# Kernel tuning notes

Hardware: AMD Instinct MI355X
Metric: run time of the kernel (lower is better)

Reference implementation:

```python
import jax, jax.numpy as jnp
import numpy as np

B, S, D, H, DFF, NL, VOCAB, SRC = 16, 128, 768, 12, 3072, 6, 32000, 256


def _pe_table():
    pos = np.arange(S)[:, None].astype(np.float32)
    div = np.exp(np.arange(0, D, 2).astype(np.float32) * (-np.log(10000.0) / D))
    pe = np.zeros((S, D), np.float32)
    pe[:, 0::2] = np.sin(pos * div)
    pe[:, 1::2] = np.cos(pos * div)
    return jnp.asarray(pe)


def _ln(x, a, b, eps=1e-6):
    m = jnp.mean(x, axis=-1, keepdims=True)
    v = jnp.mean((x - m) ** 2, axis=-1, keepdims=True)
    return a * (x - m) / jnp.sqrt(v + eps) + b


def _mha(q_in, k_in, v_in, mask, Wq, bq, Wk, bk, Wv, bv, Wo, bo):
    Bq, Sq, Dm = q_in.shape
    Sk = k_in.shape[1]
    dk = Dm // H
    q = (q_in @ Wq + bq).reshape(Bq, Sq, H, dk).transpose(0, 2, 1, 3)
    k = (k_in @ Wk + bk).reshape(Bq, Sk, H, dk).transpose(0, 2, 1, 3)
    v = (v_in @ Wv + bv).reshape(Bq, Sk, H, dk).transpose(0, 2, 1, 3)
    s = jnp.einsum('bhqd,bhkd->bhqk', q, k) / jnp.sqrt(jnp.float32(dk))
    if mask is not None:
        s = jnp.where(mask == 0, jnp.float32(-1e9), s)
    a = jax.nn.softmax(s, axis=-1)
    o = jnp.einsum('bhqk,bhkd->bhqd', a, v).transpose(0, 2, 1, 3).reshape(Bq, Sq, Dm)
    return o @ Wo + bo


def _combined_mask(trg):
    # Vectorized, faithful replica of create_combined_mask (incl. its cumulative
    # cross-batch zeroing: for j in 0..B-2, if padding_start[j]!=0 zero rows
    # >= padding_start[j] of ALL batches b >= j).
    b, s = trg.shape
    is_pad = (trg == 0)
    haspad = jnp.any(is_pad, axis=1)
    start = jnp.where(haspad, jnp.argmax(is_pad, axis=1), 0)  # first pad idx, 0 if none
    c = jnp.where(start == 0, s + 1, start)                   # sentinel = never cut
    cmin = jax.lax.cummin(c)
    r = cmin[jnp.minimum(jnp.arange(b), b - 2)]               # effective cutoff per batch
    look = jnp.tril(jnp.ones((s, s), jnp.float32))
    keep = (jnp.arange(s)[None, :] < r[:, None]).astype(jnp.float32)  # (B,S) rows kept
    return (look[None] * keep[:, :, None])[:, None]           # (B,1,S,S)


def setup_inputs():
    key = jax.random.key(0)
    ks = jax.random.split(key, 16)
    tok = jax.random.randint(ks[0], (B, S), 1, VOCAB)
    lens = jax.random.randint(ks[1], (B,), S // 2, S + 1)
    trg = jnp.where(jnp.arange(S)[None, :] < lens[:, None], tok, 0).astype(jnp.int32)
    e_outputs = jax.random.normal(ks[2], (B, SRC, D), dtype=jnp.float32)
    src_mask = jax.random.randint(ks[3], (B, 1, 1, SRC), 0, 2).at[..., 0].set(1).astype(jnp.int32)
    w = lambda k, shape: (jax.random.normal(k, shape) * 0.02).astype(jnp.float32)
    emb = (jax.random.normal(ks[4], (VOCAB, D)) * 0.1).astype(jnp.float32).at[0].set(0.0)
    return {
        'trg': trg, 'e_outputs': e_outputs, 'src_mask': src_mask,
        'emb': emb,
        'y_param': jax.random.normal(ks[5], (S, D), dtype=jnp.float32),
        'pe_alpha': jnp.float32(1.0),
        'Wq': w(ks[6], (NL, 3, D, D)), 'Wk': w(ks[7], (NL, 3, D, D)),
        'Wv': w(ks[8], (NL, 3, D, D)), 'Wo': w(ks[9], (NL, 3, D, D)),
        'bq': jnp.zeros((NL, 3, D)), 'bk': jnp.zeros((NL, 3, D)),
        'bv': jnp.zeros((NL, 3, D)), 'bo': jnp.zeros((NL, 3, D)),
        'W1': w(ks[10], (NL, D, DFF)), 'b1': jnp.zeros((NL, DFF)),
        'W2': w(ks[11], (NL, DFF, D)), 'b2': jnp.zeros((NL, D)),
        'ln_a': jnp.ones((NL, 5, D)), 'ln_b': jnp.zeros((NL, 5, D)),
        'final_a': jnp.ones((D,)), 'final_b': jnp.zeros((D,)),
    }


def reference(trg, e_outputs, src_mask, emb, y_param, pe_alpha, Wq, Wk, Wv, Wo,
              bq, bk, bv, bo, W1, b1, W2, b2, ln_a, ln_b, final_a, final_b):
    x = emb[trg] + pe_alpha * _pe_table()            # embedding + scaled PE
    y = jnp.broadcast_to(y_param, (trg.shape[0],) + y_param.shape)
    trg_mask = _combined_mask(trg)
    for i in range(Wq.shape[0]):
        x2 = _ln(x, ln_a[i, 0], ln_b[i, 0])
        x = x + _mha(x2, x2, x2, trg_mask, Wq[i, 0], bq[i, 0], Wk[i, 0], bk[i, 0], Wv[i, 0], bv[i, 0], Wo[i, 0], bo[i, 0])
        y2 = _ln(y, ln_a[i, 1], ln_b[i, 1])
        y = y + _mha(y2, e_outputs, e_outputs, src_mask, Wq[i, 1], bq[i, 1], Wk[i, 1], bk[i, 1], Wv[i, 1], bv[i, 1], Wo[i, 1], bo[i, 1])
        x2 = _ln(x, ln_a[i, 2], ln_b[i, 2])
        y3 = _ln(y, ln_a[i, 3], ln_b[i, 3])
        x = x + _mha(x2, y3, y3, None, Wq[i, 2], bq[i, 2], Wk[i, 2], bk[i, 2], Wv[i, 2], bv[i, 2], Wo[i, 2], bo[i, 2])
        x2 = _ln(x, ln_a[i, 4], ln_b[i, 4])
        x = x + jnp.maximum(x2 @ W1[i] + b1[i], 0.0) @ W2[i] + b2[i]
    return _ln(x, final_a, final_b)
```

## Files before the change

### kernel.cpp

```cpp
#include <hip/hip_runtime.h>
#include <math.h>

#define BB 16
#define SS 128
#define DD 768
#define HH 12
#define DKK 64
#define DFFF 3072
#define NLL 6
#define SRCC 256

typedef short bf16x8 __attribute__((ext_vector_type(8)));
typedef float f32x4 __attribute__((ext_vector_type(4)));
typedef unsigned short us8 __attribute__((ext_vector_type(8)));
typedef unsigned short us4 __attribute__((ext_vector_type(4)));

__device__ __forceinline__ unsigned short f2bf(float f) {
  unsigned int u = __builtin_bit_cast(unsigned int, f);
  u = (u + 0x7fff + ((u >> 16) & 1)) >> 16;
  return (unsigned short)u;
}

#define GLOADLDS16(gp, lp)                                              \
  __builtin_amdgcn_global_load_lds(                                     \
      (const __attribute__((address_space(1))) void*)(gp),              \
      (__attribute__((address_space(3))) void*)(lp), 16, 0, 0)

__global__ void embjoint_k(const int* __restrict__ trg, const float* __restrict__ emb,
                           const float* __restrict__ alpha,
                           const float* __restrict__ yp,
                           float* __restrict__ x, float* __restrict__ y) {
  int idx = blockIdx.x * blockDim.x + threadIdx.x;
  int c = idx % (DD / 4);
  int r = idx / (DD / 4);
  if (r >= BB * SS) return;
  int s = r % SS;
  if (blockIdx.y == 0) {
    float al = alpha[0];
    float4 e = *(const float4*)(emb + (size_t)trg[r] * DD + c * 4);
    float coef = -logf(10000.0f) / (float)DD;
    float div0 = expf((float)(4 * c) * coef);
    float div1 = expf((float)(4 * c + 2) * coef);
    float s0, c0, s1, c1;
    sincosf((float)s * div0, &s0, &c0);
    sincosf((float)s * div1, &s1, &c1);
    float4 o;
    o.x = e.x + al * s0; o.y = e.y + al * c0;
    o.z = e.z + al * s1; o.w = e.w + al * c1;
    *(float4*)(x + (size_t)r * DD + c * 4) = o;
  } else {
    *(float4*)(y + (size_t)r * DD + c * 4) = *(const float4*)(yp + (size_t)s * DD + c * 4);
  }
}

__global__ void mb_k(const int* __restrict__ trg, int* __restrict__ rbuf,
                     const float* __restrict__ bq, const float* __restrict__ bk,
                     const float* __restrict__ bv, float* __restrict__ bqkv1,
                     float* __restrict__ bkv2, float* __restrict__ bqkv3) {
  int t = threadIdx.x;
  if (blockIdx.x == 0) {
    __shared__ int first[BB];
    if (t < BB) first[t] = 0x7fffffff;
    __syncthreads();
    int b = t >> 4, p0 = (t & 15) * 8;
    int loc = 0x7fffffff;
#pragma unroll
    for (int i = 0; i < 8; i++) {
      if (trg[b * SS + p0 + i] == 0) { loc = p0 + i; break; }
    }
    atomicMin(&first[b], loc);
    __syncthreads();
    if (t == 0) {
      int cmin = 0x7fffffff;
      int cm[BB];
      for (int bb = 0; bb < BB; bb++) {
        int start = (first[bb] == 0x7fffffff) ? 0 : first[bb];
        int c = (start == 0) ? (SS + 1) : start;
        cmin = min(cmin, c);
        cm[bb] = cmin;
      }
      for (int bb = 0; bb < BB; bb++) rbuf[bb] = cm[min(bb, BB - 2)];
    }
    return;
  }
  int i = (blockIdx.x - 1) * 256 + t;
  if (i >= NLL * 6144) return;
  int l = i / 6144, j = i - l * 6144;
  if (j < 2304) {
    int s = j / 768, c = j - s * 768;
    const float* src = (s == 0) ? bq : (s == 1 ? bk : bv);
    bqkv1[l * 2304 + j] = src[(l * 3 + 0) * 768 + c];
  } else if (j < 3840) {
    int jj = j - 2304;
    int s = jj / 768, c = jj - s * 768;
    bkv2[l * 1536 + jj] = ((s == 0) ? bk : bv)[(l * 3 + 1) * 768 + c];
  } else {
    int jj = j - 3840;
    int s = jj / 768, c = jj - s * 768;
    const float* src = (s == 0) ? bq : (s == 1 ? bk : bv);
    bqkv3[l * 2304 + jj] = src[(l * 3 + 2) * 768 + c];
  }
}

__global__ __launch_bounds__(256) void ln_k(const float* __restrict__ x,
                                            const float* __restrict__ ga,
                                            const float* __restrict__ gb,
                                            float* __restrict__ out) {
  __shared__ float sm[8];
  int row = blockIdx.x;
  int t = threadIdx.x;
  const float* xr = x + (size_t)row * DD;
  float v0 = xr[t], v1 = xr[t + 256], v2 = xr[t + 512];
  float s = v0 + v1 + v2;
#pragma unroll
  for (int o = 32; o > 0; o >>= 1) s += __shfl_down(s, o);
  if ((t & 63) == 0) sm[t >> 6] = s;
  __syncthreads();
  float mean = (sm[0] + sm[1] + sm[2] + sm[3]) * (1.0f / (float)DD);
  float d0 = v0 - mean, d1 = v1 - mean, d2 = v2 - mean;
  float q = d0 * d0 + d1 * d1 + d2 * d2;
#pragma unroll
  for (int o = 32; o > 0; o >>= 1) q += __shfl_down(q, o);
  if ((t & 63) == 0) sm[4 + (t >> 6)] = q;
  __syncthreads();
  float var = (sm[4] + sm[5] + sm[6] + sm[7]) * (1.0f / (float)DD);
  float inv = 1.0f / sqrtf(var + 1e-6f);
  float* orow = out + (size_t)row * DD;
  orow[t]       = ga[t] * d0 * inv + gb[t];
  orow[t + 256] = ga[t + 256] * d1 * inv + gb[t + 256];
  orow[t + 512] = ga[t + 512] * d2 * inv + gb[t + 512];
}

__device__ __forceinline__ void lnb_body(const float* __restrict__ xr,
                                         const float* __restrict__ ga,
                                         const float* __restrict__ gb,
                                         unsigned short* __restrict__ orow,
                                         float* sm, int t) {
  float v0 = xr[t], v1 = xr[t + 256], v2 = xr[t + 512];
  float s = v0 + v1 + v2;
#pragma unroll
  for (int o = 32; o > 0; o >>= 1) s += __shfl_down(s, o);
  if ((t & 63) == 0) sm[t >> 6] = s;
  __syncthreads();
  float mean = (sm[0] + sm[1] + sm[2] + sm[3]) * (1.0f / (float)DD);
  float d0 = v0 - mean, d1 = v1 - mean, d2 = v2 - mean;
  float q = d0 * d0 + d1 * d1 + d2 * d2;
#pragma unroll
  for (int o = 32; o > 0; o >>= 1) q += __shfl_down(q, o);
  if ((t & 63) == 0) sm[4 + (t >> 6)] = q;
  __syncthreads();
  float var = (sm[4] + sm[5] + sm[6] + sm[7]) * (1.0f / (float)DD);
  float inv = 1.0f / sqrtf(var + 1e-6f);
  orow[t]       = f2bf(ga[t] * d0 * inv + gb[t]);
  orow[t + 256] = f2bf(ga[t + 256] * d1 * inv + gb[t + 256]);
  orow[t + 512] = f2bf(ga[t + 512] * d2 * inv + gb[t + 512]);
}

__global__ __launch_bounds__(256) void lnb_k(const float* __restrict__ x,
                                             const float* __restrict__ ga,
                                             const float* __restrict__ gb,
                                             unsigned short* __restrict__ out) {
  __shared__ float sm[8];
  int row = blockIdx.x;
  lnb_body(x + (size_t)row * DD, ga, gb, out + (size_t)row * DD, sm, threadIdx.x);
}

__global__ __launch_bounds__(256) void lnb2_k(const float* __restrict__ x,
                                              const float* __restrict__ y,
                                              const float* __restrict__ gax,
                                              const float* __restrict__ gbx,
                                              const float* __restrict__ gay,
                                              const float* __restrict__ gby,
                                              unsigned short* __restrict__ ox,
                                              unsigned short* __restrict__ oy) {
  __shared__ float sm[8];
  int row = blockIdx.x;
  if (row < BB * SS)
    lnb_body(x + (size_t)row * DD, gax, gbx, ox + (size_t)row * DD, sm, threadIdx.x);
  else {
    row -= BB * SS;
    lnb_body(y + (size_t)row * DD, gay, gby, oy + (size_t)row * DD, sm, threadIdx.x);
  }
}

__device__ __forceinline__ void tr_tile64(const float* __restrict__ s,
                                          unsigned short* __restrict__ d,
                                          int K, int N, int k0, int n0,
                                          float (*tl)[69], int t) {
#pragma unroll
  for (int i = 0; i < 4; i++) {
    int c = t + i * 256;
    int row = c >> 4, c4 = (c & 15) * 4;
    float4 v = *(const float4*)(s + (size_t)(k0 + row) * N + n0 + c4);
    tl[row][c4 + 0] = v.x; tl[row][c4 + 1] = v.y;
    tl[row][c4 + 2] = v.z; tl[row][c4 + 3] = v.w;
  }
  __syncthreads();
#pragma unroll
  for (int i = 0; i < 2; i++) {
    int c = t + i * 256;
    int n = c >> 3, kc = c & 7;
    us8 o;
#pragma unroll
    for (int j = 0; j < 8; j++) o[j] = f2bf(tl[kc * 8 + j][n]);
    *(us8*)(d + (size_t)(n0 + n) * K + k0 + kc * 8) = o;
  }
}

__global__ __launch_bounds__(256) void wtx_k(
    const float* __restrict__ Wq, const float* __restrict__ Wk,
    const float* __restrict__ Wv, const float* __restrict__ Wo,
    const float* __restrict__ W1, const float* __restrict__ W2,
    const float* __restrict__ e_out,
    unsigned short* __restrict__ wqkv1A, unsigned short* __restrict__ wq2A,
    unsigned short* __restrict__ wkv2A, unsigned short* __restrict__ wqkv3A,
    unsigned short* __restrict__ wotA,
    unsigned short* __restrict__ w1tA, unsigned short* __restrict__ w2tA,
    unsigned short* __restrict__ eob) {
  __shared__ float tl[64][69];
  const size_t M1 = (size_t)DD * DD;
  int bid = blockIdx.x;
  int t = threadIdx.x;
  if (bid < 10368) {
    int mat = bid / 144, rem = bid % 144;
    int kt = rem / 12, nt = rem % 12;
    int l = mat / 12, m = mat % 12;
    size_t s3 = (size_t)l * 3 * M1;
    const float* s;
    unsigned short* d;
    switch (m) {
      case 0:  s = Wq + s3;          d = wqkv1A + l * 3 * M1;          break;
      case 1:  s = Wk + s3;          d = wqkv1A + l * 3 * M1 + M1;     break;
      case 2:  s = Wv + s3;          d = wqkv1A + l * 3 * M1 + 2 * M1; break;
      case 3:  s = Wq + s3 + M1;     d = wq2A + l * M1;                break;
      case 4:  s = Wk + s3 + M1;     d = wkv2A + l * 2 * M1;           break;
      case 5:  s = Wv + s3 + M1;     d = wkv2A + l * 2 * M1 + M1;      break;
      case 6:  s = Wq + s3 + 2 * M1; d = wqkv3A + l * 3 * M1;          break;
      case 7:  s = Wk + s3 + 2 * M1; d = wqkv3A + l * 3 * M1 + M1;     break;
      case 8:  s = Wv + s3 + 2 * M1; d = wqkv3A + l * 3 * M1 + 2 * M1; break;
      case 9:  s = Wo + s3;          d = wotA + l * 3 * M1;            break;
      case 10: s = Wo + s3 + M1;     d = wotA + l * 3 * M1 + M1;       break;
      default: s = Wo + s3 + 2 * M1; d = wotA + l * 3 * M1 + 2 * M1;   break;
    }
    tr_tile64(s, d, DD, DD, kt * 64, nt * 64, tl, t);
  } else if (bid < 13824) {
    int idx = bid - 10368;
    int l = idx / 576, rem = idx % 576;
    int kt = rem / 48, nt = rem % 48;
    tr_tile64(W1 + (size_t)l * DD * DFFF, w1tA + (size_t)l * DD * DFFF,
              DD, DFFF, kt * 64, nt * 64, tl, t);
  } else if (bid < 17280) {
    int idx = bid - 13824;
    int l = idx / 576, rem = idx % 576;
    int kt = rem / 12, nt = rem % 12;
    tr_tile64(W2 + (size_t)l * DFFF * DD, w2tA + (size_t)l * DFFF * DD,
              DFFF, DD, kt * 64, nt * 64, tl, t);
  } else {
    size_t base = (size_t)(bid - 17280) * 2048 + (size_t)t * 8;
    float4 a = *(const float4*)(e_out + base);
    float4 b = *(const float4*)(e_out + base + 4);
    us8 o;
    o[0] = f2bf(a.x); o[1] = f2bf(a.y); o[2] = f2bf(a.z); o[3] = f2bf(a.w);
    o[4] = f2bf(b.x); o[5] = f2bf(b.y); o[6] = f2bf(b.z); o[7] = f2bf(b.w);
    *(us8*)(eob + base) = o;
  }
}

#define GEMM_BODY64(BM, A, Bt, m0, n0, KK)                                    \
  constexpr int FM = (BM) / 32;                                               \
  constexpr int HB = (BM) / 2;                                                \
  int wave = t >> 6, lane = t & 63;                                           \
  int wm = wave >> 1, wn = wave & 1;                                          \
  int l15 = lane & 15, lhi = lane >> 4;                                       \
  f32x4 acc[FM][2] = {};                                                      \
  int aRow = t >> 2, aC8 = (t & 3) * 8;                                       \
  const unsigned short* Ab = (A) + (size_t)(m0) * (KK) + aC8;                 \
  const unsigned short* Bb = (Bt) + (size_t)(n0) * (KK) + aC8;                \
  int aOff0 = (wm * HB + l15) * 32 + lhi * 8;                                 \
  int bOff0 = (wn * 32 + l15) * 32 + lhi * 8;                                 \
  for (int k0 = 0; k0 < (KK); k0 += 64) {                                     \
    _Pragma("unroll")                                                         \
    for (int p = 0; p < 2; p++) {                                             \
      _Pragma("unroll")                                                       \
      for (int h = 0; h < (BM) / 64; h++)                                     \
        GLOADLDS16(Ab + (size_t)(h * 64 + aRow) * (KK) + k0 + p * 32,         \
                   As + p * ((BM) * 32) + h * 2048 + wave * 512);             \
      GLOADLDS16(Bb + (size_t)aRow * (KK) + k0 + p * 32,                      \
                 Bs + p * 2048 + wave * 512);                                 \
    }                                                                         \
    __syncthreads();                                                          \
    _Pragma("unroll")                                                         \
    for (int p = 0; p < 2; p++) {                                             \
      bf16x8 aF[FM], bF[2];                                                   \
      _Pragma("unroll")                                                       \
      for (int fm = 0; fm < FM; fm++)                                         \
        aF[fm] = *(const bf16x8*)(As + p * ((BM) * 32) + aOff0 + fm * 16 * 32);\
      _Pragma("unroll")                                                       \
      for (int fn = 0; fn < 2; fn++)                                          \
        bF[fn] = *(const bf16x8*)(Bs + p * 2048 + bOff0 + fn * 16 * 32);      \
      _Pragma("unroll")                                                       \
      for (int fm = 0; fm < FM; fm++)                                         \
        _Pragma("unroll")                                                     \
        for (int fn = 0; fn < 2; fn++)                                        \
          acc[fm][fn] = __builtin_amdgcn_mfma_f32_16x16x32_bf16(              \
              aF[fm], bF[fn], acc[fm][fn], 0, 0, 0);                          \
    }                                                                         \
    __syncthreads();                                                          \
  }                                                                           \
  int lcol = l15, lrow4 = lhi * 4;

__device__ __forceinline__ void hm_store(unsigned short* hd, int sh, int vt,
                                         int rowb, int colr, const f32x4& a,
                                         float bv) {
  int hh = colr >> 6, dd = colr & 63;
  int bb = rowb >> sh, ssb = rowb & ((1 << sh) - 1);
  if (vt) {
    size_t idx = (((size_t)bb * HH + hh) * 64 + dd) * (size_t)(1 << sh) + ssb;
    us4 pk;
#pragma unroll
    for (int r = 0; r < 4; r++) pk[r] = f2bf(a[r] + bv);
    *(us4*)(hd + idx) = pk;
  } else {
    size_t base = ((((size_t)bb * HH + hh) << sh) + ssb) * 64 + dd;
#pragma unroll
    for (int r = 0; r < 4; r++) hd[base + (size_t)r * 64] = f2bf(a[r] + bv);
  }
}

template <int BM>
__global__ __launch_bounds__(256) void mgemm_k(
    const unsigned short* __restrict__ A0, const unsigned short* __restrict__ A1,
    const unsigned short* __restrict__ Bt, const float* __restrict__ bias,
    const float* __restrict__ res, void* __restrict__ C,
    unsigned short* __restrict__ hd0, unsigned short* __restrict__ hd1,
    unsigned short* __restrict__ hd2,
    int sh0, int sh1, int sh2, int M, int N, int K, int flags, int vtbits) {
  __shared__ unsigned short As[2 * BM * 32];
  __shared__ unsigned short Bs[2 * 64 * 32];
  int t = threadIdx.x;
  int m0 = blockIdx.y * BM, n0 = blockIdx.x * 64;
  int seg = n0 / 768;
  const unsigned short* A = (seg == 0) ? A0 : A1;
  GEMM_BODY64(BM, A, Bt, m0, n0, K)
  bool hm = (flags & 4) != 0;
  unsigned short* hd = nullptr;
  int sh = 0, segBase = seg * 768, vtseg = 0;
  if (hm) {
    hd = (seg == 0) ? hd0 : (seg == 1 ? hd1 : hd2);
    sh = (seg == 0) ? sh0 : (seg == 1 ? sh1 : sh2);
    vtseg = (vtbits >> seg) & 1;
  }
#pragma unroll
  for (int fm = 0; fm < FM; fm++) {
#pragma unroll
    for (int fn = 0; fn < 2; fn++) {
      int col = n0 + wn * 32 + fn * 16 + lcol;
      float bv = bias[col];
      int rowb = m0 + wm * HB + fm * 16 + lrow4;
      if (hm) {
        hm_store(hd, sh, vtseg, rowb, col - segBase, acc[fm][fn], bv);
      } else {
#pragma unroll
        for (int r = 0; r < 4; r++) {
          int row = rowb + r;
          float v = acc[fm][fn][r] + bv;
          size_t idx = (size_t)row * N + col;
          if (res) v += res[idx];
          if (flags & 1) v = fmaxf(v, 0.f);
          if (flags & 2) ((unsigned short*)C)[idx] = f2bf(v);
          else ((float*)C)[idx] = v;
        }
      }
    }
  }
}

__global__ __launch_bounds__(256) void kv2all_k(
    const unsigned short* __restrict__ eob, const unsigned short* __restrict__ wkv2A,
    const float* __restrict__ bkv2,
    unsigned short* __restrict__ khb2A, unsigned short* __restrict__ vthb2A) {
  __shared__ unsigned short As[2 * 128 * 32];
  __shared__ unsigned short Bs[2 * 64 * 32];
  const size_t M1 = (size_t)DD * DD;
  const size_t KVS = (size_t)BB * HH * SRCC * DKK;
  int t = threadIdx.x;
  int flat = blockIdx.x;
  int nf = (flat & 7) * 576 + (flat >> 3);
  int bx = nf % 24;
  int rem = nf / 24;
  int by = rem & 31;
  int l = rem >> 5;
  int m0 = by * 128, n0 = bx * 64;
  const unsigned short* Bt = wkv2A + (size_t)l * 2 * M1;
  const float* bias = bkv2 + l * 1536;
  GEMM_BODY64(128, eob, Bt, m0, n0, 768)
  int seg = n0 / 768;
  unsigned short* hd = (seg == 0) ? khb2A + (size_t)l * KVS : vthb2A + (size_t)l * KVS;
  int segBase = seg * 768;
#pragma unroll
  for (int fm = 0; fm < FM; fm++) {
#pragma unroll
    for (int fn = 0; fn < 2; fn++) {
      int col = n0 + wn * 32 + fn * 16 + lcol;
      int rowb = m0 + wm * HB + fm * 16 + lrow4;
      hm_store(hd, 8, seg, rowb, col - segBase, acc[fm][fn], bias[col]);
    }
  }
}

__global__ __launch_bounds__(256) void qkvq_k(
    const unsigned short* __restrict__ x2b, const unsigned short* __restrict__ y1b,
    const unsigned short* __restrict__ Bqkv, const unsigned short* __restrict__ Bq2,
    const float* __restrict__ bias1, const float* __restrict__ bias2,
    unsigned short* __restrict__ qhb, unsigned short* __restrict__ khb,
    unsigned short* __restrict__ vthb, unsigned short* __restrict__ qhb2) {
  __shared__ unsigned short As[2 * 128 * 32];
  __shared__ unsigned short Bs[2 * 64 * 32];
  int t = threadIdx.x;
  int bid = blockIdx.x;
  bool j1 = bid >= 576;
  int bx, by;
  const unsigned short *A, *Bt;
  const float* bias;
  if (!j1) { bx = bid % 36; by = bid / 36; A = x2b; Bt = Bqkv; bias = bias1; }
  else { int b2 = bid - 576; bx = b2 % 12; by = b2 / 12; A = y1b; Bt = Bq2; bias = bias2; }
  int m0 = by * 128, n0 = bx * 64;
  GEMM_BODY64(128, A, Bt, m0, n0, 768)
  int seg = j1 ? 0 : (n0 / 768);
  unsigned short* hd = j1 ? qhb2 : (seg == 0 ? qhb : (seg == 1 ? khb : vthb));
  int vt = (!j1 && seg == 2) ? 1 : 0;
  int segBase = seg * 768;
#pragma unroll
  for (int fm = 0; fm < FM; fm++) {
#pragma unroll
    for (int fn = 0; fn < 2; fn++) {
      int col = n0 + wn * 32 + fn * 16 + lcol;
      int rowb = m0 + wm * HB + fm * 16 + lrow4;
      hm_store(hd, 7, vt, rowb, col - segBase, acc[fm][fn], bias[col]);
    }
  }
}

__global__ __launch_bounds__(256) void wob_k(
    const unsigned short* __restrict__ ctx1b, const unsigned short* __restrict__ ctx2b,
    const unsigned short* __restrict__ Bt0, const unsigned short* __restrict__ Bt1,
    const float* __restrict__ bo0, const float* __restrict__ bo1,
    float* __restrict__ x, float* __restrict__ y) {
  __shared__ unsigned short As[2 * 64 * 32];
  __shared__ unsigned short Bs[2 * 64 * 32];
  int t = threadIdx.x;
  int bid = blockIdx.x;
  bool j1 = bid >= 384;
  int b2 = j1 ? bid - 384 : bid;
  int bx = b2 % 12, by = b2 / 12;
  const unsigned short* A = j1 ? ctx2b : ctx1b;
  const unsigned short* Bt = j1 ? Bt1 : Bt0;
  const float* bias = j1 ? bo1 : bo0;
  float* C = j1 ? y : x;
  int m0 = by * 64, n0 = bx * 64;
  GEMM_BODY64(64, A, Bt, m0, n0, 768)
#pragma unroll
  for (int fm = 0; fm < FM; fm++) {
#pragma unroll
    for (int fn = 0; fn < 2; fn++) {
      int col = n0 + wn * 32 + fn * 16 + lcol;
      float bv = bias[col];
      int rowb = m0 + wm * HB + fm * 16 + lrow4;
#pragma unroll
      for (int r = 0; r < 4; r++) {
        size_t idx = (size_t)(rowb + r) * DD + col;
        C[idx] += acc[fm][fn][r] + bv;
      }
    }
  }
}

template <int SK>
__device__ __forceinline__ void attn_body(
    const unsigned short* __restrict__ qh, const unsigned short* __restrict__ kh,
    const unsigned short* __restrict__ vth, unsigned short* __restrict__ ctxb,
    int mode, const int* __restrict__ rbuf, const int* __restrict__ smask,
    unsigned short* __restrict__ kvb, unsigned short* __restrict__ pbuf,
    int qhalf, int h, int b) {
  constexpr int NPH = SK / 128;
  constexpr int NF = SK / 16;
  int t = threadIdx.x;
  int wave = t >> 6, lane = t & 63;
  int l15 = lane & 15, lhi = lane >> 4;
  int qrow0 = qhalf * 64 + wave * 16;
  size_t bh = (size_t)b * HH + h;
  bf16x8 aQ[2];
#pragma unroll
  for (int ks = 0; ks < 2; ks++)
    aQ[ks] = *(const bf16x8*)(qh + (bh * SS + qrow0 + l15) * 64 + ks * 32 + lhi * 8);
  f32x4 accS[NF] = {};
  const unsigned short* kbase = kh + bh * SK * 64;
  for (int ph = 0; ph < NPH; ph++) {
    if (ph) __syncthreads();
    {
      int c0 = t * 4;
#pragma unroll
      for (int i = 0; i < 4; i++) {
        int c = c0 + i, row = c >> 3, co = (c & 7) * 8;
        *(us8*)&kvb[row * 72 + co] = *(const us8*)(kbase + (size_t)(ph * 128 + row) * 64 + co);
      }
    }
    __syncthreads();
#pragma unroll
    for (int kf = 0; kf < 8; kf++) {
      int gf = ph * 8 + kf;
#pragma unroll
      for (int ks = 0; ks < 2; ks++) {
        bf16x8 bK = *(const bf16x8*)(&kvb[(kf * 16 + l15) * 72 + ks * 32 + lhi * 8]);
        accS[gf] = __builtin_amdgcn_mfma_f32_16x16x32_bf16(aQ[ks], bK, accS[gf], 0, 0, 0);
      }
    }
  }
  int rcut = (mode == 0) ? rbuf[b] : 0;
#pragma unroll
  for (int r = 0; r < 4; r++) {
    int qg = qrow0 + lhi * 4 + r;
    float mx = -3.4e38f;
#pragma unroll
    for (int gf = 0; gf < NF; gf++) {
      int k = gf * 16 + l15;
      float s = accS[gf][r] * 0.125f;
      bool keep = true;
      if (mode == 0) keep = (k <= qg) && (qg < rcut);
      else if (mode == 1) keep = (smask[b * SRCC + k] != 0);
      s = keep ? s : -1e9f;
      accS[gf][r] = s;
      mx = fmaxf(mx, s);
    }
#pragma unroll
    for (int o = 1; o < 16; o <<= 1) mx = fmaxf(mx, __shfl_xor(mx, o));
    float sum = 0.f;
#pragma unroll
    for (int gf = 0; gf < NF; gf++) {
      float e = expf(accS[gf][r] - mx);
      accS[gf][r] = e;
      sum += e;
    }
#pragma unroll
    for (int o = 1; o < 16; o <<= 1) sum += __shfl_xor(sum, o);
    float rinv = 1.0f / sum;
#pragma unroll
    for (int gf = 0; gf < NF; gf++) accS[gf][r] *= rinv;
  }
#pragma unroll
  for (int gf = 0; gf < NF; gf++) {
#pragma unroll
    for (int r = 0; r < 4; r++) {
      int ql = wave * 16 + lhi * 4 + r;
      pbuf[ql * (SK + 8) + gf * 16 + l15] = f2bf(accS[gf][r]);
    }
  }
  __syncthreads();
  f32x4 accO[4] = {};
  const unsigned short* vbase = vth + bh * 64 * SK;
  for (int ph = 0; ph < NPH; ph++) {
    if (ph) __syncthreads();
    {
      int c0 = t * 4;
#pragma unroll
      for (int i = 0; i < 4; i++) {
        int c = c0 + i, row = c >> 4, co = (c & 15) * 8;
        *(us8*)&kvb[row * 136 + co] = *(const us8*)(vbase + (size_t)row * SK + ph * 128 + co);
      }
    }
    __syncthreads();
#pragma unroll
    for (int ks = 0; ks < 4; ks++) {
      bf16x8 aP = *(const bf16x8*)(&pbuf[(wave * 16 + l15) * (SK + 8) + ph * 128 + ks * 32 + lhi * 8]);
#pragma unroll
      for (int nf = 0; nf < 4; nf++) {
        bf16x8 bV = *(const bf16x8*)(&kvb[(nf * 16 + l15) * 136 + ks * 32 + lhi * 8]);
        accO[nf] = __builtin_amdgcn_mfma_f32_16x16x32_bf16(aP, bV, accO[nf], 0, 0, 0);
      }
    }
  }
#pragma unroll
  for (int nf = 0; nf < 4; nf++) {
#pragma unroll
    for (int r = 0; r < 4; r++) {
      int qg = qrow0 + lhi * 4 + r;
      ctxb[((size_t)b * SS + qg) * DD + h * 64 + nf * 16 + l15] = f2bf(accO[nf][r]);
    }
  }
}

template <int SK>
__global__ __launch_bounds__(256) void attn3_k(const unsigned short* __restrict__ qh,
                                               const unsigned short* __restrict__ kh,
                                               const unsigned short* __restrict__ vth,
                                               unsigned short* __restrict__ ctxb, int mode,
                                               const int* __restrict__ rbuf,
                                               const int* __restrict__ smask) {
  __shared__ unsigned short kvb[128 * 72];
  __shared__ unsigned short pbuf[64 * (SK + 8)];
  attn_body<SK>(qh, kh, vth, ctxb, mode, rbuf, smask, kvb, pbuf,
                blockIdx.x, blockIdx.y, blockIdx.z);
}

__global__ __launch_bounds__(256) void attnboth_k(
    const unsigned short* __restrict__ qh1, const unsigned short* __restrict__ kh1,
    const unsigned short* __restrict__ vth1,
    const unsigned short* __restrict__ qh2, const unsigned short* __restrict__ kh2,
    const unsigned short* __restrict__ vth2,
    unsigned short* __restrict__ ctx1b, unsigned short* __restrict__ ctx2b,
    const int* __restrict__ rbuf, const int* __restrict__ smask) {
  __shared__ unsigned short kvb[128 * 72];
  __shared__ unsigned short pbuf[64 * (SRCC + 8)];
  int bid = blockIdx.x;
  if (bid < 384) {
    int qhalf = bid & 1, rest = bid >> 1;
    int h = rest % HH, b = rest / HH;
    attn_body<SRCC>(qh2, kh2, vth2, ctx2b, 1, nullptr, smask, kvb, pbuf, qhalf, h, b);
  } else {
    int b2 = bid - 384;
    int qhalf = b2 & 1, rest = b2 >> 1;
    int h = rest % HH, b = rest / HH;
    attn_body<SS>(qh1, kh1, vth1, ctx1b, 0, rbuf, nullptr, kvb, pbuf, qhalf, h, b);
  }
}

extern "C" void kernel_launch(void* const* d_in, const int* in_sizes, int n_in,
                              void* d_out, int out_size, void* d_ws, size_t ws_size,
                              hipStream_t stream) {
  const int*   trg   = (const int*)d_in[0];
  const float* e_out = (const float*)d_in[1];
  const int*   smask = (const int*)d_in[2];
  const float* emb   = (const float*)d_in[3];
  const float* ypar  = (const float*)d_in[4];
  const float* alpha = (const float*)d_in[5];
  const float* Wq = (const float*)d_in[6];
  const float* Wk = (const float*)d_in[7];
  const float* Wv = (const float*)d_in[8];
  const float* Wo = (const float*)d_in[9];
  const float* bq = (const float*)d_in[10];
  const float* bk = (const float*)d_in[11];
  const float* bv = (const float*)d_in[12];
  const float* bo = (const float*)d_in[13];
  const float* W1 = (const float*)d_in[14];
  const float* b1 = (const float*)d_in[15];
  const float* W2 = (const float*)d_in[16];
  const float* b2 = (const float*)d_in[17];
  const float* lna = (const float*)d_in[18];
  const float* lnbp = (const float*)d_in[19];
  const float* fa = (const float*)d_in[20];
  const float* fb = (const float*)d_in[21];
  float* out = (float*)d_out;

  float* ws = (float*)d_ws;
  size_t off = 0;
  auto alloc = [&](size_t n) { float* p = ws + off; off += n; return p; };
  const size_t M1 = (size_t)DD * DD;
  const size_t KVS = (size_t)BB * HH * SRCC * DKK;
  int* rbuf  = (int*)alloc(64);
  float* x   = alloc((size_t)BB * SS * DD);
  float* y   = alloc((size_t)BB * SS * DD);
  float* bqkv1 = alloc((size_t)NLL * 2304);
  float* bkv2  = alloc((size_t)NLL * 1536);
  float* bqkv3 = alloc((size_t)NLL * 2304);
  unsigned short* qhb   = (unsigned short*)alloc((size_t)BB * HH * SS * DKK / 2);
  unsigned short* qhb2  = (unsigned short*)alloc((size_t)BB * HH * SS * DKK / 2);
  unsigned short* khb   = (unsigned short*)alloc((size_t)BB * HH * SS * DKK / 2);
  unsigned short* vthb  = (unsigned short*)alloc((size_t)BB * HH * SS * DKK / 2);
  unsigned short* khb2A  = (unsigned short*)alloc((size_t)NLL * KVS / 2);
  unsigned short* vthb2A = (unsigned short*)alloc((size_t)NLL * KVS / 2);
  unsigned short* x2b   = (unsigned short*)alloc((size_t)BB * SS * DD / 2);
  unsigned short* y3b   = (unsigned short*)alloc((size_t)BB * SS * DD / 2);
  unsigned short* ctx1b = (unsigned short*)alloc((size_t)BB * SS * DD / 2);
  unsigned short* ctx2b = (unsigned short*)alloc((size_t)BB * SS * DD / 2);
  unsigned short* midb  = (unsigned short*)alloc((size_t)BB * SS * DFFF / 2);
  unsigned short* eob   = (unsigned short*)alloc((size_t)BB * SRCC * DD / 2);
  unsigned short* wqkv1A = (unsigned short*)alloc((size_t)NLL * 3 * M1 / 2);
  unsigned short* wq2A   = (unsigned short*)alloc((size_t)NLL * M1 / 2);
  unsigned short* wkv2A  = (unsigned short*)alloc((size_t)NLL * 2 * M1 / 2);
  unsigned short* wqkv3A = (unsigned short*)alloc((size_t)NLL * 3 * M1 / 2);
  unsigned short* wotA   = (unsigned short*)alloc((size_t)NLL * 3 * M1 / 2);
  unsigned short* w1tA   = (unsigned short*)alloc((size_t)NLL * DD * DFFF / 2);
  unsigned short* w2tA   = (unsigned short*)alloc((size_t)NLL * DFFF * DD / 2);
  if (ws_size < off * sizeof(float)) return;

  embjoint_k<<<dim3((BB * SS * (DD / 4) + 255) / 256, 2), 256, 0, stream>>>(
      trg, emb, alpha, ypar, x, y);
  mb_k<<<1 + (NLL * 6144 + 255) / 256, 256, 0, stream>>>(trg, rbuf, bq, bk, bv,
                                                         bqkv1, bkv2, bqkv3);
  wtx_k<<<18816, 256, 0, stream>>>(Wq, Wk, Wv, Wo, W1, W2, e_out,
                                   wqkv1A, wq2A, wkv2A, wqkv3A, wotA, w1tA, w2tA, eob);
  kv2all_k<<<4608, 256, 0, stream>>>(eob, wkv2A, bkv2, khb2A, vthb2A);

  auto MG128 = [&](const unsigned short* A0, const unsigned short* A1, int M, int K,
                   const unsigned short* Bt, int N, const float* bias, const float* res,
                   void* C, unsigned short* h0, unsigned short* h1, unsigned short* h2,
                   int s0, int s1, int s2, int flags, int vtb) {
    mgemm_k<128><<<dim3(N / 64, M / 128), 256, 0, stream>>>(A0, A1, Bt, bias, res, C,
                                                            h0, h1, h2, s0, s1, s2, M, N, K, flags, vtb);
  };
  auto MG64 = [&](const unsigned short* A0, int M, int K,
                  const unsigned short* Bt, int N, const float* bias, const float* res,
                  void* C, unsigned short* h0, int s0, int flags, int vtb) {
    mgemm_k<64><<<dim3(N / 64, M / 64), 256, 0, stream>>>(A0, A0, Bt, bias, res, C,
                                                          h0, nullptr, nullptr, s0, 0, 0, M, N, K, flags, vtb);
  };
  const dim3 agrid(SS / 64, HH, BB);

  for (int l = 0; l < NLL; l++) {
    const float* lA = lna + (size_t)l * 5 * DD;
    const float* lB = lnbp + (size_t)l * 5 * DD;
    lnb2_k<<<2 * BB * SS, 256, 0, stream>>>(x, y, lA, lB, lA + DD, lB + DD, x2b, y3b);
    qkvq_k<<<768, 256, 0, stream>>>(x2b, y3b, wqkv1A + l * 3 * M1, wq2A + l * M1,
                                    bqkv1 + l * 2304, bq + ((size_t)l * 3 + 1) * DD,
                                    qhb, khb, vthb, qhb2);
    attnboth_k<<<768, 256, 0, stream>>>(qhb, khb, vthb,
                                        qhb2, khb2A + l * KVS, vthb2A + l * KVS,
                                        ctx1b, ctx2b, rbuf, smask);
    wob_k<<<768, 256, 0, stream>>>(ctx1b, ctx2b, wotA + l * 3 * M1, wotA + l * 3 * M1 + M1,
                                   bo + (size_t)l * 3 * DD, bo + ((size_t)l * 3 + 1) * DD, x, y);
    lnb2_k<<<2 * BB * SS, 256, 0, stream>>>(x, y, lA + 2 * DD, lB + 2 * DD,
                                            lA + 3 * DD, lB + 3 * DD, x2b, y3b);
    MG128(x2b, y3b, BB * SS, DD, wqkv3A + l * 3 * M1, 2304, bqkv3 + l * 2304, nullptr,
          nullptr, qhb, khb, vthb, 7, 7, 7, 4, 0b100);
    attn3_k<SS><<<agrid, 256, 0, stream>>>(qhb, khb, vthb, ctx1b, 2, nullptr, nullptr);
    MG64(ctx1b, BB * SS, DD, wotA + l * 3 * M1 + 2 * M1, DD, bo + ((size_t)l * 3 + 2) * DD,
         x, x, nullptr, 0, 0, 0);
    lnb_k<<<BB * SS, 256, 0, stream>>>(x, lA + 4 * DD, lB + 4 * DD, x2b);
    MG128(x2b, x2b, BB * SS, DD, w1tA + (size_t)l * DD * DFFF, DFFF, b1 + (size_t)l * DFFF,
          nullptr, midb, nullptr, nullptr, nullptr, 0, 0, 0, 3, 0);
    MG64(midb, BB * SS, DFFF, w2tA + (size_t)l * DFFF * DD, DD, b2 + (size_t)l * DD, x, x,
         nullptr, 0, 0, 0);
  }
  ln_k<<<BB * SS, 256, 0, stream>>>(x, fa, fb, out);
}
```

Before: 1.378 ms.

## Merge embedding and mask/bias prep kernels into weight-transpose kernel; remap block order

Folds the embedding+positional-encoding kernel and the mask/bias-packing kernel into the big weight-transpose launch as extra block ranges, removing two kernel launches and their serialization. It also permutes the transpose block index (interleaving by 8) so consecutive hardware blocks touch different matrices, presumably to spread memory traffic across channels. This adds branch complexity and shared-memory use to one kernel.

Result: faster. 1.348 ms (median of 2 runs) (-2.1%).

```diff
diff --git a/kernel.cpp b/kernel.cpp
--- a/kernel.cpp
+++ b/kernel.cpp
@@ -25,82 +25,6 @@
   __builtin_amdgcn_global_load_lds(                                     \
       (const __attribute__((address_space(1))) void*)(gp),              \
       (__attribute__((address_space(3))) void*)(lp), 16, 0, 0)
-
-__global__ void embjoint_k(const int* __restrict__ trg, const float* __restrict__ emb,
-                           const float* __restrict__ alpha,
-                           const float* __restrict__ yp,
-                           float* __restrict__ x, float* __restrict__ y) {
-  int idx = blockIdx.x * blockDim.x + threadIdx.x;
-  int c = idx % (DD / 4);
-  int r = idx / (DD / 4);
-  if (r >= BB * SS) return;
-  int s = r % SS;
-  if (blockIdx.y == 0) {
-    float al = alpha[0];
-    float4 e = *(const float4*)(emb + (size_t)trg[r] * DD + c * 4);
-    float coef = -logf(10000.0f) / (float)DD;
-    float div0 = expf((float)(4 * c) * coef);
-    float div1 = expf((float)(4 * c + 2) * coef);
-    float s0, c0, s1, c1;
-    sincosf((float)s * div0, &s0, &c0);
-    sincosf((float)s * div1, &s1, &c1);
-    float4 o;
-    o.x = e.x + al * s0; o.y = e.y + al * c0;
-    o.z = e.z + al * s1; o.w = e.w + al * c1;
-    *(float4*)(x + (size_t)r * DD + c * 4) = o;
-  } else {
-    *(float4*)(y + (size_t)r * DD + c * 4) = *(const float4*)(yp + (size_t)s * DD + c * 4);
-  }
-}
-
-__global__ void mb_k(const int* __restrict__ trg, int* __restrict__ rbuf,
-                     const float* __restrict__ bq, const float* __restrict__ bk,
-                     const float* __restrict__ bv, float* __restrict__ bqkv1,
-                     float* __restrict__ bkv2, float* __restrict__ bqkv3) {
-  int t = threadIdx.x;
-  if (blockIdx.x == 0) {
-    __shared__ int first[BB];
-    if (t < BB) first[t] = 0x7fffffff;
-    __syncthreads();
-    int b = t >> 4, p0 = (t & 15) * 8;
-    int loc = 0x7fffffff;
-#pragma unroll
-    for (int i = 0; i < 8; i++) {
-      if (trg[b * SS + p0 + i] == 0) { loc = p0 + i; break; }
-    }
-    atomicMin(&first[b], loc);
-    __syncthreads();
-    if (t == 0) {
-      int cmin = 0x7fffffff;
-      int cm[BB];
-      for (int bb = 0; bb < BB; bb++) {
-        int start = (first[bb] == 0x7fffffff) ? 0 : first[bb];
-        int c = (start == 0) ? (SS + 1) : start;
-        cmin = min(cmin, c);
-        cm[bb] = cmin;
-      }
-      for (int bb = 0; bb < BB; bb++) rbuf[bb] = cm[min(bb, BB - 2)];
-    }
-    return;
-  }
-  int i = (blockIdx.x - 1) * 256 + t;
-  if (i >= NLL * 6144) return;
-  int l = i / 6144, j = i - l * 6144;
-  if (j < 2304) {
-    int s = j / 768, c = j - s * 768;
-    const float* src = (s == 0) ? bq : (s == 1 ? bk : bv);
-    bqkv1[l * 2304 + j] = src[(l * 3 + 0) * 768 + c];
-  } else if (j < 3840) {
-    int jj = j - 2304;
-    int s = jj / 768, c = jj - s * 768;
-    bkv2[l * 1536 + jj] = ((s == 0) ? bk : bv)[(l * 3 + 1) * 768 + c];
-  } else {
-    int jj = j - 3840;
-    int s = jj / 768, c = jj - s * 768;
-    const float* src = (s == 0) ? bq : (s == 1 ? bk : bv);
-    bqkv3[l * 2304 + jj] = src[(l * 3 + 2) * 768 + c];
-  }
-}
 
 __global__ __launch_bounds__(256) void ln_k(const float* __restrict__ x,
                                             const float* __restrict__ ga,
@@ -216,53 +140,130 @@
     unsigned short* __restrict__ wkv2A, unsigned short* __restrict__ wqkv3A,
     unsigned short* __restrict__ wotA,
     unsigned short* __restrict__ w1tA, unsigned short* __restrict__ w2tA,
-    unsigned short* __restrict__ eob) {
+    unsigned short* __restrict__ eob,
+    const int* __restrict__ trg, const float* __restrict__ emb,
+    const float* __restrict__ alpha, const float* __restrict__ yp,
+    float* __restrict__ x, float* __restrict__ y,
+    int* __restrict__ rbuf,
+    const float* __restrict__ bq, const float* __restrict__ bk,
+    const float* __restrict__ bv, float* __restrict__ bqkv1,
+    float* __restrict__ bkv2, float* __restrict__ bqkv3) {
   __shared__ float tl[64][69];
   const size_t M1 = (size_t)DD * DD;
-  int bid = blockIdx.x;
+  int rawbid = blockIdx.x;
   int t = threadIdx.x;
-  if (bid < 10368) {
-    int mat = bid / 144, rem = bid % 144;
-    int kt = rem / 12, nt = rem % 12;
-    int l = mat / 12, m = mat % 12;
-    size_t s3 = (size_t)l * 3 * M1;
-    const float* s;
-    unsigned short* d;
-    switch (m) {
-      case 0:  s = Wq + s3;          d = wqkv1A + l * 3 * M1;          break;
-      case 1:  s = Wk + s3;          d = wqkv1A + l * 3 * M1 + M1;     break;
-      case 2:  s = Wv + s3;          d = wqkv1A + l * 3 * M1 + 2 * M1; break;
-      case 3:  s = Wq + s3 + M1;     d = wq2A + l * M1;                break;
-      case 4:  s = Wk + s3 + M1;     d = wkv2A + l * 2 * M1;           break;
-      case 5:  s = Wv + s3 + M1;     d = wkv2A + l * 2 * M1 + M1;      break;
-      case 6:  s = Wq + s3 + 2 * M1; d = wqkv3A + l * 3 * M1;          break;
-      case 7:  s = Wk + s3 + 2 * M1; d = wqkv3A + l * 3 * M1 + M1;     break;
-      case 8:  s = Wv + s3 + 2 * M1; d = wqkv3A + l * 3 * M1 + 2 * M1; break;
-      case 9:  s = Wo + s3;          d = wotA + l * 3 * M1;            break;
-      case 10: s = Wo + s3 + M1;     d = wotA + l * 3 * M1 + M1;       break;
-      default: s = Wo + s3 + 2 * M1; d = wotA + l * 3 * M1 + 2 * M1;   break;
-    }
-    tr_tile64(s, d, DD, DD, kt * 64, nt * 64, tl, t);
-  } else if (bid < 13824) {
-    int idx = bid - 10368;
-    int l = idx / 576, rem = idx % 576;
-    int kt = rem / 48, nt = rem % 48;
-    tr_tile64(W1 + (size_t)l * DD * DFFF, w1tA + (size_t)l * DD * DFFF,
-              DD, DFFF, kt * 64, nt * 64, tl, t);
-  } else if (bid < 17280) {
-    int idx = bid - 13824;
-    int l = idx / 576, rem = idx % 576;
-    int kt = rem / 12, nt = rem % 12;
-    tr_tile64(W2 + (size_t)l * DFFF * DD, w2tA + (size_t)l * DFFF * DD,
-              DFFF, DD, kt * 64, nt * 64, tl, t);
+  if (rawbid < 18816) {
+    int bid = (rawbid & 7) * 2352 + (rawbid >> 3);
+    if (bid < 10368) {
+      int mat = bid / 144, rem = bid % 144;
+      int kt = rem / 12, nt = rem % 12;
+      int l = mat / 12, m = mat % 12;
+      size_t s3 = (size_t)l * 3 * M1;
+      const float* s;
+      unsigned short* d;
+      switch (m) {
+        case 0:  s = Wq + s3;          d = wqkv1A + l * 3 * M1;          break;
+        case 1:  s = Wk + s3;          d = wqkv1A + l * 3 * M1 + M1;     break;
+        case 2:  s = Wv + s3;          d = wqkv1A + l * 3 * M1 + 2 * M1; break;
+        case 3:  s = Wq + s3 + M1;     d = wq2A + l * M1;                break;
+        case 4:  s = Wk + s3 + M1;     d = wkv2A + l * 2 * M1;           break;
+        case 5:  s = Wv + s3 + M1;     d = wkv2A + l * 2 * M1 + M1;      break;
+        case 6:  s = Wq + s3 + 2 * M1; d = wqkv3A + l * 3 * M1;          break;
+        case 7:  s = Wk + s3 + 2 * M1; d = wqkv3A + l * 3 * M1 + M1;     break;
+        case 8:  s = Wv + s3 + 2 * M1; d = wqkv3A + l * 3 * M1 + 2 * M1; break;
+        case 9:  s = Wo + s3;          d = wotA + l * 3 * M1;            break;
+        case 10: s = Wo + s3 + M1;     d = wotA + l * 3 * M1 + M1;       break;
+        default: s = Wo + s3 + 2 * M1; d = wotA + l * 3 * M1 + 2 * M1;   break;
+      }
+      tr_tile64(s, d, DD, DD, kt * 64, nt * 64, tl, t);
+    } else if (bid < 13824) {
+      int idx = bid - 10368;
+      int l = idx / 576, rem = idx % 576;
+      int kt = rem / 48, nt = rem % 48;
+      tr_tile64(W1 + (size_t)l * DD * DFFF, w1tA + (size_t)l * DD * DFFF,
+                DD, DFFF, kt * 64, nt * 64, tl, t);
+    } else if (bid < 17280) {
+      int idx = bid - 13824;
+      int l = idx / 576, rem = idx % 576;
+      int kt = rem / 12, nt = rem % 12;
+      tr_tile64(W2 + (size_t)l * DFFF * DD, w2tA + (size_t)l * DFFF * DD,
+                DFFF, DD, kt * 64, nt * 64, tl, t);
+    } else {
+      size_t base = (size_t)(bid - 17280) * 2048 + (size_t)t * 8;
+      float4 a = *(const float4*)(e_out + base);
+      float4 b = *(const float4*)(e_out + base + 4);
+      us8 o;
+      o[0] = f2bf(a.x); o[1] = f2bf(a.y); o[2] = f2bf(a.z); o[3] = f2bf(a.w);
+      o[4] = f2bf(b.x); o[5] = f2bf(b.y); o[6] = f2bf(b.z); o[7] = f2bf(b.w);
+      *(us8*)(eob + base) = o;
+    }
+  } else if (rawbid < 21888) {
+    int z = rawbid - 18816;
+    int half = (z >= 1536) ? 1 : 0;
+    int idx = (z - half * 1536) * 256 + t;
+    int c = idx % (DD / 4);
+    int r = idx / (DD / 4);
+    int s = r % SS;
+    if (half == 0) {
+      float al = alpha[0];
+      float4 e = *(const float4*)(emb + (size_t)trg[r] * DD + c * 4);
+      float coef = -logf(10000.0f) / (float)DD;
+      float div0 = expf((float)(4 * c) * coef);
+      float div1 = expf((float)(4 * c + 2) * coef);
+      float s0, c0, s1, c1;
+      sincosf((float)s * div0, &s0, &c0);
+      sincosf((float)s * div1, &s1, &c1);
+      float4 o;
+      o.x = e.x + al * s0; o.y = e.y + al * c0;
+      o.z = e.z + al * s1; o.w = e.w + al * c1;
+      *(float4*)(x + (size_t)r * DD + c * 4) = o;
+    } else {
+      *(float4*)(y + (size_t)r * DD + c * 4) = *(const float4*)(yp + (size_t)s * DD + c * 4);
+    }
   } else {
-    size_t base = (size_t)(bid - 17280) * 2048 + (size_t)t * 8;
-    float4 a = *(const float4*)(e_out + base);
-    float4 b = *(const float4*)(e_out + base + 4);
-    us8 o;
-    o[0] = f2bf(a.x); o[1] = f2bf(a.y); o[2] = f2bf(a.z); o[3] = f2bf(a.w);
-    o[4] = f2bf(b.x); o[5] = f2bf(b.y); o[6] = f2bf(b.z); o[7] = f2bf(b.w);
-    *(us8*)(eob + base) = o;
+    int mbid = rawbid - 21888;
+    if (mbid == 0) {
+      __shared__ int first[BB];
+      if (t < BB) first[t] = 0x7fffffff;
+      __syncthreads();
+      int b = t >> 4, p0 = (t & 15) * 8;
+      int loc = 0x7fffffff;
+#pragma unroll
+      for (int i = 0; i < 8; i++) {
+        if (trg[b * SS + p0 + i] == 0) { loc = p0 + i; break; }
+      }
+      atomicMin(&first[b], loc);
+      __syncthreads();
+      if (t == 0) {
+        int cmin = 0x7fffffff;
+        int cm[BB];
+        for (int bb = 0; bb < BB; bb++) {
+          int start = (first[bb] == 0x7fffffff) ? 0 : first[bb];
+          int c = (start == 0) ? (SS + 1) : start;
+          cmin = min(cmin, c);
+          cm[bb] = cmin;
+        }
+        for (int bb = 0; bb < BB; bb++) rbuf[bb] = cm[min(bb, BB - 2)];
+      }
+      return;
+    }
+    int i = (mbid - 1) * 256 + t;
+    if (i >= NLL * 6144) return;
+    int l = i / 6144, j = i - l * 6144;
+    if (j < 2304) {
+      int s = j / 768, c = j - s * 768;
+      const float* src = (s == 0) ? bq : (s == 1 ? bk : bv);
+      bqkv1[l * 2304 + j] = src[(l * 3 + 0) * 768 + c];
+    } else if (j < 3840) {
+      int jj = j - 2304;
+      int s = jj / 768, c = jj - s * 768;
+      bkv2[l * 1536 + jj] = ((s == 0) ? bk : bv)[(l * 3 + 1) * 768 + c];
+    } else {
+      int jj = j - 3840;
+      int s = jj / 768, c = jj - s * 768;
+      const float* src = (s == 0) ? bq : (s == 1 ? bk : bv);
+      bqkv3[l * 2304 + jj] = src[(l * 3 + 2) * 768 + c];
+    }
   }
 }
 
@@ -683,12 +684,10 @@
   unsigned short* w2tA   = (unsigned short*)alloc((size_t)NLL * DFFF * DD / 2);
   if (ws_size < off * sizeof(float)) return;
 
-  embjoint_k<<<dim3((BB * SS * (DD / 4) + 255) / 256, 2), 256, 0, stream>>>(
-      trg, emb, alpha, ypar, x, y);
-  mb_k<<<1 + (NLL * 6144 + 255) / 256, 256, 0, stream>>>(trg, rbuf, bq, bk, bv,
-                                                         bqkv1, bkv2, bqkv3);
-  wtx_k<<<18816, 256, 0, stream>>>(Wq, Wk, Wv, Wo, W1, W2, e_out,
-                                   wqkv1A, wq2A, wkv2A, wqkv3A, wotA, w1tA, w2tA, eob);
+  wtx_k<<<22033, 256, 0, stream>>>(Wq, Wk, Wv, Wo, W1, W2, e_out,
+                                   wqkv1A, wq2A, wkv2A, wqkv3A, wotA, w1tA, w2tA, eob,
+                                   trg, emb, alpha, ypar, x, y, rbuf,
+                                   bq, bk, bv, bqkv1, bkv2, bqkv3);
   kv2all_k<<<4608, 256, 0, stream>>>(eob, wkv2A, bkv2, khb2A, vthb2A);
 
   auto MG128 = [&](const unsigned short* A0, const unsigned short* A1, int M, int K,
```
